# Optimization experiments

Measured on AMD Instinct MI355X. Metric: run time of the kernel, lower is better.

Reference implementation:

```python
import jax, jax.numpy as jnp
import numpy as np

N_NODES = 100000
N_EDGES = 3200000
D_IN = 256
D_OUT = 256


def setup_inputs() -> dict:
    key = jax.random.key(0)
    k1, k2, k3, k4, k5, k6 = jax.random.split(key, 6)
    features = jax.random.normal(k1, (N_NODES, D_IN), dtype=jnp.float32)
    adj_row = jax.random.randint(k2, (N_EDGES,), 0, N_NODES, dtype=jnp.int32)
    adj_col = jax.random.randint(k3, (N_EDGES,), 0, N_NODES, dtype=jnp.int32)
    adj_val = jax.random.uniform(k4, (N_EDGES,), dtype=jnp.float32)
    # xavier-normal with gain 0.02 (reset_parameters_xavier)
    w_std = 0.02 * np.sqrt(2.0 / (D_IN + D_OUT))
    weight = jax.random.normal(k5, (D_IN, D_OUT), dtype=jnp.float32) * w_std
    b_std = 0.02 * np.sqrt(2.0 / (1 + D_OUT))
    bias = jax.random.normal(k6, (1, D_OUT), dtype=jnp.float32) * b_std
    return {"features": features, "adj_row": adj_row, "adj_col": adj_col,
            "adj_val": adj_val, "weight": weight, "bias": bias}


def reference(features, adj_row, adj_col, adj_val, weight, bias):
    # h = X @ W  : [N, D_out]
    h = jnp.matmul(features, weight)
    # SpMM: out[i] = sum_{e: row[e]==i} val[e] * h[col[e]]
    msgs = adj_val[:, None] * h[adj_col]          # [E, D_out]
    agg = jax.ops.segment_sum(msgs, adj_row, num_segments=N_NODES)
    return agg + bias
```

## Files before the change

kernel.cpp:

```cpp
#include <hip/hip_runtime.h>
#include <hip/hip_bf16.h>

typedef float  f32x4  __attribute__((ext_vector_type(4)));
typedef short  s16x8  __attribute__((ext_vector_type(8)));
typedef unsigned short u16x4 __attribute__((ext_vector_type(4)));
typedef unsigned short u16x8 __attribute__((ext_vector_type(8)));

constexpr int N_NODES = 100000;
constexpr int N_EDGES = 3200000;
constexpr int D = 256;

constexpr size_t OFF_H        = 0;
constexpr size_t OFF_COUNTS   = 51200000;
constexpr size_t OFF_ROWSTART = 51600000;
constexpr size_t OFF_BSUM     = 52000256;
constexpr size_t OFF_BOFF     = 52000768;
constexpr size_t OFF_WT       = 52001280;
constexpr size_t OFF_PACKED   = 52132352;
constexpr int SCAN_BLK = 98;

__device__ inline unsigned short f2bf(float f) {
  __hip_bfloat16 h = __float2bfloat16(f);
  return *reinterpret_cast<unsigned short*>(&h);
}

__global__ __launch_bounds__(256)
void wt_cast(const float* __restrict__ W, unsigned short* __restrict__ Wt) {
  __shared__ float Ws[32][33];
  const int bx = blockIdx.x & 7, by = blockIdx.x >> 3;
  const int k0 = by * 32, j0 = bx * 32;
  const int t = threadIdx.x;
  const int tr = t >> 3, tc = (t & 7) * 4;
  f32x4 v = *reinterpret_cast<const f32x4*>(W + (size_t)(k0 + tr) * D + j0 + tc);
#pragma unroll
  for (int i = 0; i < 4; ++i) Ws[tr][tc + i] = v[i];
  __syncthreads();
  u16x4 o = { f2bf(Ws[tc + 0][tr]), f2bf(Ws[tc + 1][tr]),
              f2bf(Ws[tc + 2][tr]), f2bf(Ws[tc + 3][tr]) };
  *reinterpret_cast<u16x4*>(Wt + (size_t)(j0 + tr) * D + k0 + tc) = o;
}

__global__ __launch_bounds__(256, 2)
void gemm_mfma(const float* __restrict__ X, const unsigned short* __restrict__ Wt,
               unsigned short* __restrict__ Hb) {
  __shared__ char As[128 * 64];
  __shared__ char Bs[256 * 64];

  const int t    = threadIdx.x;
  const int l    = t & 63;
  const int w    = t >> 6;
  const int row0 = blockIdx.x * 128;
  const int m_base = w * 32;

  f32x4 acc[2][16];
#pragma unroll
  for (int mi = 0; mi < 2; ++mi)
#pragma unroll
    for (int ni = 0; ni < 16; ++ni) acc[mi][ni] = (f32x4){0.f, 0.f, 0.f, 0.f};

  for (int kc = 0; kc < D; kc += 32) {
#pragma unroll
    for (int i = 0; i < 4; ++i) {
      const int lin = i * 256 + t;
      const int r = lin >> 3, g = lin & 7;
      int row = row0 + r; if (row >= N_NODES) row = N_NODES - 1;
      f32x4 v = *reinterpret_cast<const f32x4*>(X + (size_t)row * D + kc + g * 4);
      u16x4 o = { f2bf(v[0]), f2bf(v[1]), f2bf(v[2]), f2bf(v[3]) };
      *reinterpret_cast<u16x4*>(As + r * 64 + ((g * 8) ^ ((r & 3) << 4))) = o;
    }
#pragma unroll
    for (int i = 0; i < 4; ++i) {
      const int lin = i * 256 + t;
      const int j = lin >> 2, g = lin & 3;
      u16x8 v = *reinterpret_cast<const u16x8*>(Wt + (size_t)j * D + kc + g * 8);
      *reinterpret_cast<u16x8*>(Bs + j * 64 + ((g * 16) ^ ((j & 3) << 4))) = v;
    }
    __syncthreads();

    s16x8 a[2];
#pragma unroll
    for (int mi = 0; mi < 2; ++mi) {
      const int r = m_base + mi * 16 + (l & 15);
      a[mi] = *reinterpret_cast<const s16x8*>(
          As + r * 64 + (((l >> 4) * 16) ^ ((r & 3) << 4)));
    }
#pragma unroll
    for (int ni = 0; ni < 16; ++ni) {
      const int j = ni * 16 + (l & 15);
      s16x8 b = *reinterpret_cast<const s16x8*>(
          Bs + j * 64 + (((l >> 4) * 16) ^ ((j & 3) << 4)));
      acc[0][ni] = __builtin_amdgcn_mfma_f32_16x16x32_bf16(a[0], b, acc[0][ni], 0, 0, 0);
      acc[1][ni] = __builtin_amdgcn_mfma_f32_16x16x32_bf16(a[1], b, acc[1][ni], 0, 0, 0);
    }
    __syncthreads();
  }

#pragma unroll
  for (int mi = 0; mi < 2; ++mi)
#pragma unroll
    for (int ni = 0; ni < 16; ++ni)
#pragma unroll
      for (int r = 0; r < 4; ++r) {
        const int row = row0 + m_base + mi * 16 + ((l >> 4) << 2) + r;
        if (row < N_NODES)
          Hb[(size_t)row * D + ni * 16 + (l & 15)] = f2bf(acc[mi][ni][r]);
      }
}

__global__ __launch_bounds__(256)
void hist_rows(const int* __restrict__ arow, int* __restrict__ counts) {
  for (int i = blockIdx.x * 256 + threadIdx.x; i < N_EDGES; i += gridDim.x * 256)
    atomicAdd(&counts[arow[i]], 1);
}

__global__ __launch_bounds__(256)
void scan_block_sums(const int* __restrict__ counts, int* __restrict__ bsum) {
  __shared__ int sd[256];
  const int b = blockIdx.x, t = threadIdx.x;
  const int base = b * 1024 + t * 4;
  int s = 0;
#pragma unroll
  for (int j = 0; j < 4; ++j) { int idx = base + j; if (idx < N_NODES) s += counts[idx]; }
  sd[t] = s; __syncthreads();
  for (int off = 128; off > 0; off >>= 1) {
    if (t < off) sd[t] += sd[t + off];
    __syncthreads();
  }
  if (t == 0) bsum[b] = sd[0];
}

__global__ __launch_bounds__(128)
void scan_bsums(const int* __restrict__ bsum, int* __restrict__ boff,
                int* __restrict__ row_start) {
  __shared__ int sd[128];
  const int t = threadIdx.x;
  int v = (t < SCAN_BLK) ? bsum[t] : 0;
  sd[t] = v; __syncthreads();
  for (int off = 1; off < 128; off <<= 1) {
    int x = (t >= off) ? sd[t - off] : 0;
    __syncthreads();
    sd[t] += x;
    __syncthreads();
  }
  if (t < SCAN_BLK) boff[t] = sd[t] - v;
  if (t == 0) row_start[N_NODES] = N_EDGES;
}

__global__ __launch_bounds__(256)
void scan_write(const int* __restrict__ counts, const int* __restrict__ boff,
                int* __restrict__ row_start) {
  __shared__ int sd[256];
  const int b = blockIdx.x, t = threadIdx.x;
  const int base = b * 1024 + t * 4;
  int v[4];
#pragma unroll
  for (int j = 0; j < 4; ++j) v[j] = (base + j < N_NODES) ? counts[base + j] : 0;
  int l0 = 0, l1 = v[0], l2 = v[0] + v[1], l3 = v[0] + v[1] + v[2];
  int s = l3 + v[3];
  sd[t] = s; __syncthreads();
  for (int off = 1; off < 256; off <<= 1) {
    int x = (t >= off) ? sd[t - off] : 0;
    __syncthreads();
    sd[t] += x;
    __syncthreads();
  }
  const int o = boff[b] + sd[t] - s;
  if (base + 0 < N_NODES) row_start[base + 0] = o + l0;
  if (base + 1 < N_NODES) row_start[base + 1] = o + l1;
  if (base + 2 < N_NODES) row_start[base + 2] = o + l2;
  if (base + 3 < N_NODES) row_start[base + 3] = o + l3;
}

__global__ __launch_bounds__(256)
void bin_edges(const int* __restrict__ arow, const int* __restrict__ acol,
               const float* __restrict__ aval, int* __restrict__ counts,
               const int* __restrict__ row_start, int2* __restrict__ packed) {
  for (int i = blockIdx.x * 256 + threadIdx.x; i < N_EDGES; i += gridDim.x * 256) {
    const int r = arow[i];
    const int old = atomicSub(&counts[r], 1);
    packed[row_start[r] + old - 1] = make_int2(acol[i], __float_as_int(aval[i]));
  }
}

__device__ inline f32x4 bf4_to_f4(u16x4 h) {
  f32x4 r;
#pragma unroll
  for (int j = 0; j < 4; ++j) r[j] = __uint_as_float(((unsigned)h[j]) << 16);
  return r;
}

__global__ __launch_bounds__(256)
void row_reduce(const int* __restrict__ row_start, const int2* __restrict__ packed,
                const unsigned short* __restrict__ Hb, const float* __restrict__ bias,
                float* __restrict__ out) {
  const int row = blockIdx.x * 4 + (threadIdx.x >> 6);
  const int l = threadIdx.x & 63;
  if (row >= N_NODES) return;
  const int s = row_start[row];
  const int e = row_start[row + 1];

  f32x4 a0 = {0.f,0.f,0.f,0.f}, a1 = a0, a2 = a0, a3 = a0;
  int i = s;
  for (; i + 4 <= e; i += 4) {
    const int2 p0 = packed[i],     p1 = packed[i + 1];
    const int2 p2 = packed[i + 2], p3 = packed[i + 3];
    const f32x4 h0 = bf4_to_f4(*reinterpret_cast<const u16x4*>(Hb + (size_t)p0.x * D + l * 4));
    const f32x4 h1 = bf4_to_f4(*reinterpret_cast<const u16x4*>(Hb + (size_t)p1.x * D + l * 4));
    const f32x4 h2 = bf4_to_f4(*reinterpret_cast<const u16x4*>(Hb + (size_t)p2.x * D + l * 4));
    const f32x4 h3 = bf4_to_f4(*reinterpret_cast<const u16x4*>(Hb + (size_t)p3.x * D + l * 4));
    const float v0 = __int_as_float(p0.y), v1 = __int_as_float(p1.y);
    const float v2 = __int_as_float(p2.y), v3 = __int_as_float(p3.y);
#pragma unroll
    for (int j = 0; j < 4; ++j) {
      a0[j] += v0 * h0[j]; a1[j] += v1 * h1[j];
      a2[j] += v2 * h2[j]; a3[j] += v3 * h3[j];
    }
  }
  for (; i < e; ++i) {
    const int2 p = packed[i];
    const f32x4 h = bf4_to_f4(*reinterpret_cast<const u16x4*>(Hb + (size_t)p.x * D + l * 4));
    const float v = __int_as_float(p.y);
#pragma unroll
    for (int j = 0; j < 4; ++j) a0[j] += v * h[j];
  }
  const f32x4 b = *reinterpret_cast<const f32x4*>(bias + l * 4);
  f32x4 o;
#pragma unroll
  for (int j = 0; j < 4; ++j) o[j] = (a0[j] + a1[j]) + (a2[j] + a3[j]) + b[j];
  *reinterpret_cast<f32x4*>(out + (size_t)row * D + l * 4) = o;
}

extern "C" void kernel_launch(void* const* d_in, const int* in_sizes, int n_in,
                              void* d_out, int out_size, void* d_ws, size_t ws_size,
                              hipStream_t stream) {
  const float* X    = (const float*)d_in[0];
  const int*   arow = (const int*)  d_in[1];
  const int*   acol = (const int*)  d_in[2];
  const float* aval = (const float*)d_in[3];
  const float* W    = (const float*)d_in[4];
  const float* bias = (const float*)d_in[5];
  float* out = (float*)d_out;

  char* ws = (char*)d_ws;
  unsigned short* Hb        = (unsigned short*)(ws + OFF_H);
  int*            counts    = (int*)  (ws + OFF_COUNTS);
  int*            row_start = (int*)  (ws + OFF_ROWSTART);
  int*            bsum      = (int*)  (ws + OFF_BSUM);
  int*            boff      = (int*)  (ws + OFF_BOFF);
  unsigned short* Wt        = (unsigned short*)(ws + OFF_WT);
  int2*           packed    = (int2*) (ws + OFF_PACKED);

  wt_cast<<<64, 256, 0, stream>>>(W, Wt);
  gemm_mfma<<<(N_NODES + 127) / 128, 256, 0, stream>>>(X, Wt, Hb);

  hipMemsetAsync(counts, 0, N_NODES * sizeof(int), stream);
  hist_rows<<<2048, 256, 0, stream>>>(arow, counts);
  scan_block_sums<<<SCAN_BLK, 256, 0, stream>>>(counts, bsum);
  scan_bsums<<<1, 128, 0, stream>>>(bsum, boff, row_start);
  scan_write<<<SCAN_BLK, 256, 0, stream>>>(counts, boff, row_start);
  bin_edges<<<2048, 256, 0, stream>>>(arow, acol, aval, counts, row_start, packed);

  row_reduce<<<(N_NODES + 3) / 4, 256, 0, stream>>>(row_start, packed, Hb, bias, out);
}
```

Before: 718.5 us.

## Widen GEMM K-tile, vectorize edge loads, deepen SpMM gather unroll

The GEMM now stages 64-wide K chunks in LDS with an 8-way XOR swizzle, which halves the number of barrier pairs per tile. The histogram and binning kernels read row, column and value arrays as int4/float4 and issue four atomics per thread. The row-reduce gather unrolls to 8 independent edges with 8 accumulators so more Hb loads are in flight. Together these target latency and memory-level parallelism across several stages, at the cost of more LDS and registers in the GEMM and more registers in row_reduce, which may lower occupancy.

```diff
diff --git a/kernel.cpp b/kernel.cpp
--- a/kernel.cpp
+++ b/kernel.cpp
@@ -43,8 +43,8 @@
 __global__ __launch_bounds__(256, 2)
 void gemm_mfma(const float* __restrict__ X, const unsigned short* __restrict__ Wt,
                unsigned short* __restrict__ Hb) {
-  __shared__ char As[128 * 64];
-  __shared__ char Bs[256 * 64];
+  __shared__ char As[128 * 128];
+  __shared__ char Bs[256 * 128];
 
   const int t    = threadIdx.x;
   const int l    = t & 63;
@@ -58,39 +58,44 @@
 #pragma unroll
     for (int ni = 0; ni < 16; ++ni) acc[mi][ni] = (f32x4){0.f, 0.f, 0.f, 0.f};
 
-  for (int kc = 0; kc < D; kc += 32) {
-#pragma unroll
-    for (int i = 0; i < 4; ++i) {
+  for (int kc = 0; kc < D; kc += 64) {
+#pragma unroll
+    for (int i = 0; i < 8; ++i) {
       const int lin = i * 256 + t;
-      const int r = lin >> 3, g = lin & 7;
+      const int r = lin >> 4, g = lin & 15;
       int row = row0 + r; if (row >= N_NODES) row = N_NODES - 1;
       f32x4 v = *reinterpret_cast<const f32x4*>(X + (size_t)row * D + kc + g * 4);
       u16x4 o = { f2bf(v[0]), f2bf(v[1]), f2bf(v[2]), f2bf(v[3]) };
-      *reinterpret_cast<u16x4*>(As + r * 64 + ((g * 8) ^ ((r & 3) << 4))) = o;
-    }
-#pragma unroll
-    for (int i = 0; i < 4; ++i) {
+      *reinterpret_cast<u16x4*>(As + r * 128 + ((g * 8) ^ ((r & 7) << 4))) = o;
+    }
+#pragma unroll
+    for (int i = 0; i < 8; ++i) {
       const int lin = i * 256 + t;
-      const int j = lin >> 2, g = lin & 3;
+      const int j = lin >> 3, g = lin & 7;
       u16x8 v = *reinterpret_cast<const u16x8*>(Wt + (size_t)j * D + kc + g * 8);
-      *reinterpret_cast<u16x8*>(Bs + j * 64 + ((g * 16) ^ ((j & 3) << 4))) = v;
-    }
-    __syncthreads();
-
-    s16x8 a[2];
-#pragma unroll
-    for (int mi = 0; mi < 2; ++mi) {
-      const int r = m_base + mi * 16 + (l & 15);
-      a[mi] = *reinterpret_cast<const s16x8*>(
-          As + r * 64 + (((l >> 4) * 16) ^ ((r & 3) << 4)));
-    }
+      *reinterpret_cast<u16x8*>(Bs + j * 128 + ((g * 16) ^ ((j & 7) << 4))) = v;
+    }
+    __syncthreads();
+
+    s16x8 a[2][2];
+#pragma unroll
+    for (int mi = 0; mi < 2; ++mi)
+#pragma unroll
+      for (int kk = 0; kk < 2; ++kk) {
+        const int r = m_base + mi * 16 + (l & 15);
+        a[mi][kk] = *reinterpret_cast<const s16x8*>(
+            As + r * 128 + ((kk * 64 + (l >> 4) * 16) ^ ((r & 7) << 4)));
+      }
 #pragma unroll
     for (int ni = 0; ni < 16; ++ni) {
       const int j = ni * 16 + (l & 15);
-      s16x8 b = *reinterpret_cast<const s16x8*>(
-          Bs + j * 64 + (((l >> 4) * 16) ^ ((j & 3) << 4)));
-      acc[0][ni] = __builtin_amdgcn_mfma_f32_16x16x32_bf16(a[0], b, acc[0][ni], 0, 0, 0);
-      acc[1][ni] = __builtin_amdgcn_mfma_f32_16x16x32_bf16(a[1], b, acc[1][ni], 0, 0, 0);
+#pragma unroll
+      for (int kk = 0; kk < 2; ++kk) {
+        s16x8 b = *reinterpret_cast<const s16x8*>(
+            Bs + j * 128 + ((kk * 64 + (l >> 4) * 16) ^ ((j & 7) << 4)));
+        acc[0][ni] = __builtin_amdgcn_mfma_f32_16x16x32_bf16(a[0][kk], b, acc[0][ni], 0, 0, 0);
+        acc[1][ni] = __builtin_amdgcn_mfma_f32_16x16x32_bf16(a[1][kk], b, acc[1][ni], 0, 0, 0);
+      }
     }
     __syncthreads();
   }
@@ -109,8 +114,15 @@
 
 __global__ __launch_bounds__(256)
 void hist_rows(const int* __restrict__ arow, int* __restrict__ counts) {
-  for (int i = blockIdx.x * 256 + threadIdx.x; i < N_EDGES; i += gridDim.x * 256)
-    atomicAdd(&counts[arow[i]], 1);
+  const int4* a4 = reinterpret_cast<const int4*>(arow);
+  const int n4 = N_EDGES / 4;
+  for (int i = blockIdx.x * 256 + threadIdx.x; i < n4; i += gridDim.x * 256) {
+    const int4 r = a4[i];
+    atomicAdd(&counts[r.x], 1);
+    atomicAdd(&counts[r.y], 1);
+    atomicAdd(&counts[r.z], 1);
+    atomicAdd(&counts[r.w], 1);
+  }
 }
 
 __global__ __launch_bounds__(256)
@@ -175,10 +187,17 @@
 void bin_edges(const int* __restrict__ arow, const int* __restrict__ acol,
                const float* __restrict__ aval, int* __restrict__ counts,
                const int* __restrict__ row_start, int2* __restrict__ packed) {
-  for (int i = blockIdx.x * 256 + threadIdx.x; i < N_EDGES; i += gridDim.x * 256) {
-    const int r = arow[i];
-    const int old = atomicSub(&counts[r], 1);
-    packed[row_start[r] + old - 1] = make_int2(acol[i], __float_as_int(aval[i]));
+  const int4*   r4 = reinterpret_cast<const int4*>(arow);
+  const int4*   c4 = reinterpret_cast<const int4*>(acol);
+  const float4* v4 = reinterpret_cast<const float4*>(aval);
+  const int n4 = N_EDGES / 4;
+  for (int i = blockIdx.x * 256 + threadIdx.x; i < n4; i += gridDim.x * 256) {
+    const int4 r = r4[i]; const int4 c = c4[i]; const float4 v = v4[i];
+    int o;
+    o = atomicSub(&counts[r.x], 1); packed[row_start[r.x] + o - 1] = make_int2(c.x, __float_as_int(v.x));
+    o = atomicSub(&counts[r.y], 1); packed[row_start[r.y] + o - 1] = make_int2(c.y, __float_as_int(v.y));
+    o = atomicSub(&counts[r.z], 1); packed[row_start[r.z] + o - 1] = make_int2(c.z, __float_as_int(v.z));
+    o = atomicSub(&counts[r.w], 1); packed[row_start[r.w] + o - 1] = make_int2(c.w, __float_as_int(v.w));
   }
 }
 
@@ -199,34 +218,46 @@
   const int s = row_start[row];
   const int e = row_start[row + 1];
 
-  f32x4 a0 = {0.f,0.f,0.f,0.f}, a1 = a0, a2 = a0, a3 = a0;
+  f32x4 acc[8];
+#pragma unroll
+  for (int u = 0; u < 8; ++u) acc[u] = (f32x4){0.f, 0.f, 0.f, 0.f};
+
   int i = s;
-  for (; i + 4 <= e; i += 4) {
-    const int2 p0 = packed[i],     p1 = packed[i + 1];
-    const int2 p2 = packed[i + 2], p3 = packed[i + 3];
+  for (; i + 8 <= e; i += 8) {
+    int2 p[8];
+#pragma unroll
+    for (int u = 0; u < 8; ++u) p[u] = packed[i + u];
+#pragma unroll
+    for (int u = 0; u < 8; ++u) {
+      const f32x4 h = bf4_to_f4(
+          *reinterpret_cast<const u16x4*>(Hb + (size_t)p[u].x * D + l * 4));
+      const float v = __int_as_float(p[u].y);
+#pragma unroll
+      for (int j = 0; j < 4; ++j) acc[u][j] += v * h[j];
+    }
+  }
+  for (; i + 2 <= e; i += 2) {
+    const int2 p0 = packed[i], p1 = packed[i + 1];
     const f32x4 h0 = bf4_to_f4(*reinterpret_cast<const u16x4*>(Hb + (size_t)p0.x * D + l * 4));
     const f32x4 h1 = bf4_to_f4(*reinterpret_cast<const u16x4*>(Hb + (size_t)p1.x * D + l * 4));
-    const f32x4 h2 = bf4_to_f4(*reinterpret_cast<const u16x4*>(Hb + (size_t)p2.x * D + l * 4));
-    const f32x4 h3 = bf4_to_f4(*reinterpret_cast<const u16x4*>(Hb + (size_t)p3.x * D + l * 4));
     const float v0 = __int_as_float(p0.y), v1 = __int_as_float(p1.y);
-    const float v2 = __int_as_float(p2.y), v3 = __int_as_float(p3.y);
-#pragma unroll
-    for (int j = 0; j < 4; ++j) {
-      a0[j] += v0 * h0[j]; a1[j] += v1 * h1[j];
-      a2[j] += v2 * h2[j]; a3[j] += v3 * h3[j];
-    }
-  }
-  for (; i < e; ++i) {
+#pragma unroll
+    for (int j = 0; j < 4; ++j) { acc[0][j] += v0 * h0[j]; acc[1][j] += v1 * h1[j]; }
+  }
+  if (i < e) {
     const int2 p = packed[i];
     const f32x4 h = bf4_to_f4(*reinterpret_cast<const u16x4*>(Hb + (size_t)p.x * D + l * 4));
     const float v = __int_as_float(p.y);
 #pragma unroll
-    for (int j = 0; j < 4; ++j) a0[j] += v * h[j];
-  }
+    for (int j = 0; j < 4; ++j) acc[2][j] += v * h[j];
+  }
+
   const f32x4 b = *reinterpret_cast<const f32x4*>(bias + l * 4);
   f32x4 o;
 #pragma unroll
-  for (int j = 0; j < 4; ++j) o[j] = (a0[j] + a1[j]) + (a2[j] + a3[j]) + b[j];
+  for (int j = 0; j < 4; ++j)
+    o[j] = ((acc[0][j] + acc[1][j]) + (acc[2][j] + acc[3][j])) +
+           ((acc[4][j] + acc[5][j]) + (acc[6][j] + acc[7][j])) + b[j];
   *reinterpret_cast<f32x4*>(out + (size_t)row * D + l * 4) = o;
 }
 
```

Result: no change. 728.3 us (+1.4%).
